# Kernel tuning notes

Hardware: AMD Instinct MI355X
Metric: run time of the kernel (lower is better)

Reference implementation:

```python
import jax, jax.numpy as jnp
import numpy as np

B, C, D, TOPK = 4096, 8192, 128, 10


def calc_distmat2(x, y):
    d = (x * x).sum(-1)[:, None] + (y * y).sum(-1)[None, :] - 2.0 * (x @ y.T)
    return jnp.clip(d, 1e-12, 1e12)


def setup_inputs() -> dict:
    key = jax.random.key(0)
    k1, k2, k3 = jax.random.split(key, 3)
    x = jax.random.normal(k1, (B, D), dtype=jnp.float32)
    labels = jax.random.randint(k2, (B,), 0, C)
    # kaiming_normal_(mode='fan_out') on (C, D): fan_out = C, gain = sqrt(2)
    centers = jax.random.normal(k3, (C, D), dtype=jnp.float32) * np.float32(np.sqrt(2.0 / C))
    return {"x": x, "labels": labels, "centers": centers, "topk": TOPK}


def reference(x, labels, centers, topk):
    num_classes = centers.shape[0]
    distmat = calc_distmat2(x, centers)                      # (B, C)
    lab = labels[:, None]                                    # (B, 1)
    dist_pull = jnp.take_along_axis(distmat, lab, axis=1)[:, 0]  # (B,)
    loss_pull = dist_pull.mean()

    # mode 'exp': per-row masked topk over negatives + log-softmax over [pos, neg_topk]
    logits = -distmat                                        # (B, C)
    pos = jnp.take_along_axis(logits, lab, axis=1)           # (B, 1)
    is_pos = lab == jnp.arange(num_classes)[None, :]         # (B, C)
    neg_logits = jnp.where(is_pos, -jnp.inf, logits)
    neg_topk, _ = jax.lax.top_k(neg_logits, topk)            # (B, topk)
    cat = jnp.concatenate([pos, neg_topk], axis=1)           # (B, 1+topk)
    # -log_softmax at index 0 (the positive) per row, averaged ('ccent')
    loss = (-jax.nn.log_softmax(cat, axis=1)[:, 0]).mean()

    # center-to-center repulsion over strictly-lower-triangular pairs
    cent2cent = calc_distmat2(centers, centers)              # (C, C)
    tri = jnp.tril(jnp.ones((num_classes, num_classes), dtype=bool), -1)
    n_pairs = num_classes * (num_classes - 1) // 2
    loss_dis = -jnp.sum(jnp.where(tri, cent2cent, 0.0)) / jnp.float32(n_pairs)

    return (loss, loss_dis, cent2cent, loss_pull)
```

## Files before the change

### kernel.cpp

```cpp
#include <hip/hip_runtime.h>
#include <hip/hip_bf16.h>
#include <math.h>

#define NB 4096
#define NC 8192
#define ND 128
#define NSPLIT 16
#define CPS (NC / NSPLIT)
#define NTILES (CPS / 16)
#define XBLKS (64 * NSPLIT)

#define WS_XN 16
#define WS_CN (WS_XN + NB)
#define WS_POS (WS_CN + NC)
#define WS_PART (WS_POS + NB)
#define WS_XB (WS_PART + NB * NSPLIT * 10)
#define WS_CB (WS_XB + NB * ND / 2)

typedef __attribute__((ext_vector_type(8))) short short8v;
typedef __attribute__((ext_vector_type(4))) float f32x4;

__global__ __launch_bounds__(256) void prep_kernel(
    const float* __restrict__ x, const float* __restrict__ c, float* __restrict__ ws) {
  if (blockIdx.x == 0 && threadIdx.x < 16) ws[threadIdx.x] = 0.0f;
  int wid = threadIdx.x >> 6, lane = threadIdx.x & 63;
  int row = blockIdx.x * 4 + wid;
  const float* src;
  float* ndst;
  ushort* bdst;
  if (row < NB) {
    src = x + (size_t)row * ND;
    ndst = ws + WS_XN + row;
    bdst = (ushort*)(ws + WS_XB) + (size_t)row * ND;
  } else {
    int r = row - NB;
    src = c + (size_t)r * ND;
    ndst = ws + WS_CN + r;
    bdst = (ushort*)(ws + WS_CB) + (size_t)r * ND;
  }
  float2 v = *(const float2*)(src + lane * 2);
  __hip_bfloat16 h0 = __float2bfloat16(v.x);
  __hip_bfloat16 h1 = __float2bfloat16(v.y);
  ushort2 u;
  u.x = *(ushort*)&h0;
  u.y = *(ushort*)&h1;
  *(ushort2*)(bdst + lane * 2) = u;
  float s = fmaf(v.x, v.x, v.y * v.y);
#pragma unroll
  for (int off = 32; off; off >>= 1) s += __shfl_down(s, off, 64);
  if (lane == 0) *ndst = s;
}

#define INS10(arr, val)                          \
  {                                              \
    float _v = (val);                            \
    _Pragma("unroll") for (int _k = 0; _k < 10; ++_k) { \
      float _mx = fmaxf(arr[_k], _v);            \
      _v = fminf(arr[_k], _v);                   \
      arr[_k] = _mx;                             \
    }                                            \
  }

__global__ __launch_bounds__(256) void mega_kernel(
    const int* __restrict__ labels, float* __restrict__ ws, float* __restrict__ outmat) {
  int t = threadIdx.x;
  int w = t >> 6, l = t & 63, lo = l & 15, hi = l >> 4;
  int bid = blockIdx.x;

  if (bid < XBLKS) {
    int split = bid >> 6;
    int row = (bid & 63) * 64 + w * 16 + lo;
    int cbase = split * CPS;
    const ushort* xb = (const ushort*)(ws + WS_XB);
    const ushort* cb = (const ushort*)(ws + WS_CB);

    const ushort* xrp = xb + (size_t)row * ND + hi * 8;
    short8v xf0 = *(const short8v*)(xrp + 0);
    short8v xf1 = *(const short8v*)(xrp + 32);
    short8v xf2 = *(const short8v*)(xrp + 64);
    short8v xf3 = *(const short8v*)(xrp + 96);

    float xn = ws[WS_XN + row];
    int lab = labels[row];

    float top[10];
#pragma unroll
    for (int k = 0; k < 10; ++k) top[k] = -3.0e38f;
    float posv = -3.0e38f;

    for (int tl = 0; tl < NTILES; ++tl) {
      int c0 = cbase + tl * 16;
      const ushort* cp = cb + (size_t)(c0 + lo) * ND + hi * 8;
      short8v a0 = *(const short8v*)(cp + 0);
      short8v a1 = *(const short8v*)(cp + 32);
      short8v a2 = *(const short8v*)(cp + 64);
      short8v a3 = *(const short8v*)(cp + 96);
      f32x4 acc = {0.f, 0.f, 0.f, 0.f};
      acc = __builtin_amdgcn_mfma_f32_16x16x32_bf16(a0, xf0, acc, 0, 0, 0);
      acc = __builtin_amdgcn_mfma_f32_16x16x32_bf16(a1, xf1, acc, 0, 0, 0);
      acc = __builtin_amdgcn_mfma_f32_16x16x32_bf16(a2, xf2, acc, 0, 0, 0);
      acc = __builtin_amdgcn_mfma_f32_16x16x32_bf16(a3, xf3, acc, 0, 0, 0);

      f32x4 cn4 = *(const f32x4*)(ws + WS_CN + c0 + hi * 4);
#pragma unroll
      for (int r = 0; r < 4; ++r) {
        int cidx = c0 + hi * 4 + r;
        float dist = xn + cn4[r] - 2.0f * acc[r];
        dist = fminf(fmaxf(dist, 1e-12f), 1e12f);
        float s = -dist;
        bool isl = (cidx == lab);
        posv = isl ? s : posv;
        float se = isl ? -3.0e38f : s;
        INS10(top, se)
      }
    }

    float oth[10];
#pragma unroll
    for (int m = 16; m <= 32; m <<= 1) {
#pragma unroll
      for (int k = 0; k < 10; ++k) oth[k] = __shfl_xor(top[k], m, 64);
#pragma unroll
      for (int k = 0; k < 10; ++k) INS10(top, oth[k])
    }

    if (posv > -1.0e37f) ws[WS_POS + row] = posv;
    if (hi == 0) {
      float* dst = ws + WS_PART + ((size_t)row * NSPLIT + split) * 10;
#pragma unroll
      for (int k = 0; k < 10; ++k) dst[k] = top[k];
    }
  } else {
    int bid2 = bid - XBLKS;
    int bi = bid2 >> 6, bj = bid2 & 63;
    int wm = w >> 1, wn = w & 1;
    int rowb = bi * 128 + wm * 64;
    int colb = bj * 128 + wn * 64;
    const ushort* cb = (const ushort*)(ws + WS_CB);

    f32x4 acc[4][4];
#pragma unroll
    for (int m = 0; m < 4; ++m)
#pragma unroll
      for (int n = 0; n < 4; ++n) acc[m][n] = (f32x4){0.f, 0.f, 0.f, 0.f};

#pragma unroll
    for (int ks = 0; ks < 4; ++ks) {
      short8v af[4], bf[4];
#pragma unroll
      for (int m = 0; m < 4; ++m)
        af[m] = *(const short8v*)(cb + (size_t)(rowb + m * 16 + lo) * ND + ks * 32 + hi * 8);
#pragma unroll
      for (int n = 0; n < 4; ++n)
        bf[n] = *(const short8v*)(cb + (size_t)(colb + n * 16 + lo) * ND + ks * 32 + hi * 8);
#pragma unroll
      for (int m = 0; m < 4; ++m)
#pragma unroll
        for (int n = 0; n < 4; ++n)
          acc[m][n] = __builtin_amdgcn_mfma_f32_16x16x32_bf16(af[m], bf[n], acc[m][n], 0, 0, 0);
    }

    float cnj[4];
#pragma unroll
    for (int n = 0; n < 4; ++n) cnj[n] = ws[WS_CN + colb + n * 16 + lo];
    float tsum = 0.0f;
#pragma unroll
    for (int m = 0; m < 4; ++m) {
      f32x4 cni = *(const f32x4*)(ws + WS_CN + rowb + m * 16 + hi * 4);
#pragma unroll
      for (int n = 0; n < 4; ++n) {
#pragma unroll
        for (int rr = 0; rr < 4; ++rr) {
          int gr = rowb + m * 16 + hi * 4 + rr;
          int gc = colb + n * 16 + lo;
          float dd = cni[rr] + cnj[n] - 2.0f * acc[m][n][rr];
          dd = fminf(fmaxf(dd, 1e-12f), 1e12f);
          outmat[(size_t)gr * NC + gc] = dd;
          if (bi > bj) tsum += dd;
          else if (bi == bj) tsum += (gr > gc) ? dd : 0.0f;
        }
      }
    }

    __shared__ float red[4];
#pragma unroll
    for (int off = 32; off; off >>= 1) tsum += __shfl_down(tsum, off, 64);
    if (l == 0) red[w] = tsum;
    __syncthreads();
    if (t == 0) atomicAdd(ws + 1, red[0] + red[1] + red[2] + red[3]);
  }
}

__global__ __launch_bounds__(256) void merge_fin_kernel(float* __restrict__ ws,
                                                        float* __restrict__ out) {
  int row = blockIdx.x * 256 + threadIdx.x;
  const f32x4* part = (const f32x4*)(ws + WS_PART + (size_t)row * NSPLIT * 10);
  float top[10];
#pragma unroll
  for (int k = 0; k < 10; ++k) top[k] = -3.0e38f;
#pragma unroll
  for (int i = 0; i < NSPLIT * 10 / 4; ++i) {
    f32x4 v = part[i];
    INS10(top, v.x)
    INS10(top, v.y)
    INS10(top, v.z)
    INS10(top, v.w)
  }
  float pos = ws[WS_POS + row];
  float mx = fmaxf(pos, top[0]);
  float ssum = expf(pos - mx);
#pragma unroll
  for (int k = 0; k < 10; ++k) ssum += expf(top[k] - mx);
  float lrow = mx + logf(ssum) - pos;
  float prow = -pos;
#pragma unroll
  for (int off = 32; off; off >>= 1) {
    lrow += __shfl_down(lrow, off, 64);
    prow += __shfl_down(prow, off, 64);
  }
  if ((threadIdx.x & 63) == 0) {
    atomicAdd(ws + 0, lrow);
    atomicAdd(ws + 2, prow);
  }
  __syncthreads();
  if (threadIdx.x == 0) {
    __threadfence();
    unsigned tk = atomicAdd((unsigned int*)(ws + 3), 1u);
    if (tk == 15u) {
      float ls = atomicAdd(ws + 0, 0.0f);
      float ts = atomicAdd(ws + 1, 0.0f);
      float ps = atomicAdd(ws + 2, 0.0f);
      out[0] = ls / 4096.0f;
      out[1] = -ts / 33550336.0f;
      out[2 + (size_t)NC * NC] = ps / 4096.0f;
    }
  }
}

extern "C" void kernel_launch(void* const* d_in, const int* in_sizes, int n_in,
                              void* d_out, int out_size, void* d_ws, size_t ws_size,
                              hipStream_t stream) {
  const float* x = (const float*)d_in[0];
  const int* labels = (const int*)d_in[1];
  const float* centers = (const float*)d_in[2];
  float* out = (float*)d_out;
  float* ws = (float*)d_ws;

  hipLaunchKernelGGL(prep_kernel, dim3((NB + NC) / 4), dim3(256), 0, stream, x, centers, ws);
  hipLaunchKernelGGL(mega_kernel, dim3(XBLKS + 64 * 64), dim3(256), 0, stream, labels, ws, out + 2);
  hipLaunchKernelGGL(merge_fin_kernel, dim3(NB / 256), dim3(256), 0, stream, ws, out);
}
```

Baseline: 182.9 us.

## Split mega kernel into c2c and xloss kernels with pipelined loads and merge-insert top-k

Splits the fused kernel into two launches: a center-to-center distance kernel and an x-loss top-k kernel, each with its own register footprint. The c2c kernel swaps MFMA operand order so each lane writes four contiguous floats, giving vectorized float4 stores of the 256MB output instead of scalar ones. The xloss kernel double-buffers center fragment loads across tiles and replaces four sequential 10-wide insertions with a 4-element sorting network merged into the top-10 list. In exchange it loses the overlap between the two workloads inside one grid and adds a kernel launch.

```diff
diff --git a/kernel.cpp b/kernel.cpp
--- a/kernel.cpp
+++ b/kernel.cpp
@@ -8,7 +8,7 @@
 #define NSPLIT 16
 #define CPS (NC / NSPLIT)
 #define NTILES (CPS / 16)
-#define XBLKS (64 * NSPLIT)
+#define NEGINF -3.0e38f
 
 #define WS_XN 16
 #define WS_CN (WS_XN + NB)
@@ -61,134 +61,193 @@
     }                                            \
   }
 
-__global__ __launch_bounds__(256) void mega_kernel(
-    const int* __restrict__ labels, float* __restrict__ ws, float* __restrict__ outmat) {
+#define SW(a, b) { float _x = fmaxf(a, b); b = fminf(a, b); a = _x; }
+
+#define LOADF(d0, d1, d2, d3, IDX)                                            \
+  {                                                                           \
+    const ushort* cp_ = cb + (size_t)(cbase + (IDX) * 16 + lo) * ND + hi * 8; \
+    d0 = *(const short8v*)(cp_ + 0);                                          \
+    d1 = *(const short8v*)(cp_ + 32);                                         \
+    d2 = *(const short8v*)(cp_ + 64);                                         \
+    d3 = *(const short8v*)(cp_ + 96);                                         \
+  }
+
+#define EPILOGUE(TL, ACC, CN4)                                                \
+  {                                                                           \
+    int cb0_ = cbase + (TL) * 16 + hi * 4;                                    \
+    float a0 = -(fminf(fmaxf(xn + (CN4).x - 2.0f * (ACC)[0], 1e-12f), 1e12f));\
+    float a1 = -(fminf(fmaxf(xn + (CN4).y - 2.0f * (ACC)[1], 1e-12f), 1e12f));\
+    float a2 = -(fminf(fmaxf(xn + (CN4).z - 2.0f * (ACC)[2], 1e-12f), 1e12f));\
+    float a3 = -(fminf(fmaxf(xn + (CN4).w - 2.0f * (ACC)[3], 1e-12f), 1e12f));\
+    bool l0 = (cb0_ + 0 == lab), l1 = (cb0_ + 1 == lab),                      \
+         l2 = (cb0_ + 2 == lab), l3 = (cb0_ + 3 == lab);                      \
+    posv = l0 ? a0 : posv; posv = l1 ? a1 : posv;                             \
+    posv = l2 ? a2 : posv; posv = l3 ? a3 : posv;                             \
+    a0 = l0 ? NEGINF : a0; a1 = l1 ? NEGINF : a1;                             \
+    a2 = l2 ? NEGINF : a2; a3 = l3 ? NEGINF : a3;                             \
+    SW(a0, a1) SW(a2, a3) SW(a0, a2) SW(a1, a3) SW(a1, a2)                    \
+    float n0 = fmaxf(a0, top[0]);                                             \
+    float n1 = fmaxf(fmaxf(a1, top[1]), fminf(a0, top[0]));                   \
+    float n2 = fmaxf(fmaxf(a2, top[2]),                                       \
+                     fmaxf(fminf(a0, top[1]), fminf(a1, top[0])));            \
+    float n3 = fmaxf(fmaxf(a3, top[3]),                                       \
+                     fmaxf(fmaxf(fminf(a0, top[2]), fminf(a1, top[1])),       \
+                           fminf(a2, top[0])));                               \
+    float n4 = fmaxf(top[4], fmaxf(fmaxf(fminf(a0, top[3]), fminf(a1, top[2])), \
+                                   fmaxf(fminf(a2, top[1]), fminf(a3, top[0])))); \
+    float n5 = fmaxf(top[5], fmaxf(fmaxf(fminf(a0, top[4]), fminf(a1, top[3])), \
+                                   fmaxf(fminf(a2, top[2]), fminf(a3, top[1])))); \
+    float n6 = fmaxf(top[6], fmaxf(fmaxf(fminf(a0, top[5]), fminf(a1, top[4])), \
+                                   fmaxf(fminf(a2, top[3]), fminf(a3, top[2])))); \
+    float n7 = fmaxf(top[7], fmaxf(fmaxf(fminf(a0, top[6]), fminf(a1, top[5])), \
+                                   fmaxf(fminf(a2, top[4]), fminf(a3, top[3])))); \
+    float n8 = fmaxf(top[8], fmaxf(fmaxf(fminf(a0, top[7]), fminf(a1, top[6])), \
+                                   fmaxf(fminf(a2, top[5]), fminf(a3, top[4])))); \
+    float n9 = fmaxf(top[9], fmaxf(fmaxf(fminf(a0, top[8]), fminf(a1, top[7])), \
+                                   fmaxf(fminf(a2, top[6]), fminf(a3, top[5])))); \
+    top[0] = n0; top[1] = n1; top[2] = n2; top[3] = n3; top[4] = n4;          \
+    top[5] = n5; top[6] = n6; top[7] = n7; top[8] = n8; top[9] = n9;          \
+  }
+
+__global__ __launch_bounds__(256) void xloss_kernel(
+    const int* __restrict__ labels, float* __restrict__ ws) {
   int t = threadIdx.x;
   int w = t >> 6, l = t & 63, lo = l & 15, hi = l >> 4;
-  int bid = blockIdx.x;
-
-  if (bid < XBLKS) {
-    int split = bid >> 6;
-    int row = (bid & 63) * 64 + w * 16 + lo;
-    int cbase = split * CPS;
-    const ushort* xb = (const ushort*)(ws + WS_XB);
-    const ushort* cb = (const ushort*)(ws + WS_CB);
-
-    const ushort* xrp = xb + (size_t)row * ND + hi * 8;
-    short8v xf0 = *(const short8v*)(xrp + 0);
-    short8v xf1 = *(const short8v*)(xrp + 32);
-    short8v xf2 = *(const short8v*)(xrp + 64);
-    short8v xf3 = *(const short8v*)(xrp + 96);
-
-    float xn = ws[WS_XN + row];
-    int lab = labels[row];
-
-    float top[10];
-#pragma unroll
-    for (int k = 0; k < 10; ++k) top[k] = -3.0e38f;
-    float posv = -3.0e38f;
-
-    for (int tl = 0; tl < NTILES; ++tl) {
-      int c0 = cbase + tl * 16;
-      const ushort* cp = cb + (size_t)(c0 + lo) * ND + hi * 8;
-      short8v a0 = *(const short8v*)(cp + 0);
-      short8v a1 = *(const short8v*)(cp + 32);
-      short8v a2 = *(const short8v*)(cp + 64);
-      short8v a3 = *(const short8v*)(cp + 96);
-      f32x4 acc = {0.f, 0.f, 0.f, 0.f};
-      acc = __builtin_amdgcn_mfma_f32_16x16x32_bf16(a0, xf0, acc, 0, 0, 0);
-      acc = __builtin_amdgcn_mfma_f32_16x16x32_bf16(a1, xf1, acc, 0, 0, 0);
-      acc = __builtin_amdgcn_mfma_f32_16x16x32_bf16(a2, xf2, acc, 0, 0, 0);
-      acc = __builtin_amdgcn_mfma_f32_16x16x32_bf16(a3, xf3, acc, 0, 0, 0);
-
-      f32x4 cn4 = *(const f32x4*)(ws + WS_CN + c0 + hi * 4);
-#pragma unroll
-      for (int r = 0; r < 4; ++r) {
-        int cidx = c0 + hi * 4 + r;
-        float dist = xn + cn4[r] - 2.0f * acc[r];
-        dist = fminf(fmaxf(dist, 1e-12f), 1e12f);
-        float s = -dist;
-        bool isl = (cidx == lab);
-        posv = isl ? s : posv;
-        float se = isl ? -3.0e38f : s;
-        INS10(top, se)
+  int row = blockIdx.x * 64 + w * 16 + lo;
+  int split = blockIdx.y;
+  int cbase = split * CPS;
+
+  const ushort* xb = (const ushort*)(ws + WS_XB);
+  const ushort* cb = (const ushort*)(ws + WS_CB);
+
+  const ushort* xrp = xb + (size_t)row * ND + hi * 8;
+  short8v xf0 = *(const short8v*)(xrp + 0);
+  short8v xf1 = *(const short8v*)(xrp + 32);
+  short8v xf2 = *(const short8v*)(xrp + 64);
+  short8v xf3 = *(const short8v*)(xrp + 96);
+
+  float xn = ws[WS_XN + row];
+  int lab = labels[row];
+
+  float top[10];
+#pragma unroll
+  for (int k = 0; k < 10; ++k) top[k] = NEGINF;
+  float posv = NEGINF;
+
+  short8v pa0, pa1, pa2, pa3, qa0, qa1, qa2, qa3;
+  f32x4 cnP, cnQ;
+  LOADF(pa0, pa1, pa2, pa3, 0)
+  cnP = *(const f32x4*)(ws + WS_CN + cbase + hi * 4);
+
+  for (int tl = 0; tl < NTILES; tl += 2) {
+    LOADF(qa0, qa1, qa2, qa3, tl + 1)
+    cnQ = *(const f32x4*)(ws + WS_CN + cbase + (tl + 1) * 16 + hi * 4);
+
+    f32x4 accA = {0.f, 0.f, 0.f, 0.f};
+    accA = __builtin_amdgcn_mfma_f32_16x16x32_bf16(pa0, xf0, accA, 0, 0, 0);
+    accA = __builtin_amdgcn_mfma_f32_16x16x32_bf16(pa1, xf1, accA, 0, 0, 0);
+    accA = __builtin_amdgcn_mfma_f32_16x16x32_bf16(pa2, xf2, accA, 0, 0, 0);
+    accA = __builtin_amdgcn_mfma_f32_16x16x32_bf16(pa3, xf3, accA, 0, 0, 0);
+    f32x4 cnA = cnP;
+    int nidx = (tl + 2 < NTILES) ? tl + 2 : tl;
+    LOADF(pa0, pa1, pa2, pa3, nidx)
+    cnP = *(const f32x4*)(ws + WS_CN + cbase + nidx * 16 + hi * 4);
+
+    EPILOGUE(tl, accA, cnA)
+
+    f32x4 accB = {0.f, 0.f, 0.f, 0.f};
+    accB = __builtin_amdgcn_mfma_f32_16x16x32_bf16(qa0, xf0, accB, 0, 0, 0);
+    accB = __builtin_amdgcn_mfma_f32_16x16x32_bf16(qa1, xf1, accB, 0, 0, 0);
+    accB = __builtin_amdgcn_mfma_f32_16x16x32_bf16(qa2, xf2, accB, 0, 0, 0);
+    accB = __builtin_amdgcn_mfma_f32_16x16x32_bf16(qa3, xf3, accB, 0, 0, 0);
+    EPILOGUE(tl + 1, accB, cnQ)
+  }
+
+  float oth[10];
+#pragma unroll
+  for (int m = 16; m <= 32; m <<= 1) {
+#pragma unroll
+    for (int k = 0; k < 10; ++k) oth[k] = __shfl_xor(top[k], m, 64);
+#pragma unroll
+    for (int k = 0; k < 10; ++k) INS10(top, oth[k])
+  }
+
+  if (posv > -1.0e37f) ws[WS_POS + row] = posv;
+  if (hi == 0) {
+    float* dst = ws + WS_PART + ((size_t)row * NSPLIT + split) * 10;
+#pragma unroll
+    for (int k = 0; k < 10; ++k) dst[k] = top[k];
+  }
+}
+
+__global__ __launch_bounds__(256) void c2c_kernel(
+    float* __restrict__ ws, float* __restrict__ outmat) {
+  int bi = blockIdx.x, bj = blockIdx.y;
+  int t = threadIdx.x;
+  int w = t >> 6, l = t & 63, lo = l & 15, hi = l >> 4;
+  int wm = w >> 1, wn = w & 1;
+  int rowb = bi * 128 + wm * 64;
+  int colb = bj * 128 + wn * 64;
+  const ushort* cb = (const ushort*)(ws + WS_CB);
+
+  f32x4 acc[4][4];
+#pragma unroll
+  for (int m = 0; m < 4; ++m)
+#pragma unroll
+    for (int n = 0; n < 4; ++n) acc[m][n] = (f32x4){0.f, 0.f, 0.f, 0.f};
+
+#pragma unroll
+  for (int ks = 0; ks < 4; ++ks) {
+    short8v af[4], bf[4];
+#pragma unroll
+    for (int m = 0; m < 4; ++m)
+      af[m] = *(const short8v*)(cb + (size_t)(rowb + m * 16 + lo) * ND + ks * 32 + hi * 8);
+#pragma unroll
+    for (int n = 0; n < 4; ++n)
+      bf[n] = *(const short8v*)(cb + (size_t)(colb + n * 16 + lo) * ND + ks * 32 + hi * 8);
+#pragma unroll
+    for (int m = 0; m < 4; ++m)
+#pragma unroll
+      for (int n = 0; n < 4; ++n)
+        acc[m][n] = __builtin_amdgcn_mfma_f32_16x16x32_bf16(bf[n], af[m], acc[m][n], 0, 0, 0);
+  }
+
+  float cni[4];
+#pragma unroll
+  for (int m = 0; m < 4; ++m) cni[m] = ws[WS_CN + rowb + m * 16 + lo];
+  f32x4 cnj[4];
+#pragma unroll
+  for (int n = 0; n < 4; ++n)
+    cnj[n] = *(const f32x4*)(ws + WS_CN + colb + n * 16 + hi * 4);
+
+  float tsum = 0.0f;
+#pragma unroll
+  for (int m = 0; m < 4; ++m) {
+    int gr = rowb + m * 16 + lo;
+    float* orow = outmat + (size_t)gr * NC + colb + hi * 4;
+#pragma unroll
+    for (int n = 0; n < 4; ++n) {
+      f32x4 dd;
+#pragma unroll
+      for (int rr = 0; rr < 4; ++rr)
+        dd[rr] = fminf(fmaxf(cni[m] + cnj[n][rr] - 2.0f * acc[m][n][rr], 1e-12f), 1e12f);
+      if (bi > bj) {
+        tsum += dd[0] + dd[1] + dd[2] + dd[3];
+      } else if (bi == bj) {
+        int gc0 = colb + n * 16 + hi * 4;
+#pragma unroll
+        for (int rr = 0; rr < 4; ++rr) tsum += (gr > gc0 + rr) ? dd[rr] : 0.0f;
       }
+      *(f32x4*)(orow + n * 16) = dd;
     }
-
-    float oth[10];
-#pragma unroll
-    for (int m = 16; m <= 32; m <<= 1) {
-#pragma unroll
-      for (int k = 0; k < 10; ++k) oth[k] = __shfl_xor(top[k], m, 64);
-#pragma unroll
-      for (int k = 0; k < 10; ++k) INS10(top, oth[k])
-    }
-
-    if (posv > -1.0e37f) ws[WS_POS + row] = posv;
-    if (hi == 0) {
-      float* dst = ws + WS_PART + ((size_t)row * NSPLIT + split) * 10;
-#pragma unroll
-      for (int k = 0; k < 10; ++k) dst[k] = top[k];
-    }
-  } else {
-    int bid2 = bid - XBLKS;
-    int bi = bid2 >> 6, bj = bid2 & 63;
-    int wm = w >> 1, wn = w & 1;
-    int rowb = bi * 128 + wm * 64;
-    int colb = bj * 128 + wn * 64;
-    const ushort* cb = (const ushort*)(ws + WS_CB);
-
-    f32x4 acc[4][4];
-#pragma unroll
-    for (int m = 0; m < 4; ++m)
-#pragma unroll
-      for (int n = 0; n < 4; ++n) acc[m][n] = (f32x4){0.f, 0.f, 0.f, 0.f};
-
-#pragma unroll
-    for (int ks = 0; ks < 4; ++ks) {
-      short8v af[4], bf[4];
-#pragma unroll
-      for (int m = 0; m < 4; ++m)
-        af[m] = *(const short8v*)(cb + (size_t)(rowb + m * 16 + lo) * ND + ks * 32 + hi * 8);
-#pragma unroll
-      for (int n = 0; n < 4; ++n)
-        bf[n] = *(const short8v*)(cb + (size_t)(colb + n * 16 + lo) * ND + ks * 32 + hi * 8);
-#pragma unroll
-      for (int m = 0; m < 4; ++m)
-#pragma unroll
-        for (int n = 0; n < 4; ++n)
-          acc[m][n] = __builtin_amdgcn_mfma_f32_16x16x32_bf16(af[m], bf[n], acc[m][n], 0, 0, 0);
-    }
-
-    float cnj[4];
-#pragma unroll
-    for (int n = 0; n < 4; ++n) cnj[n] = ws[WS_CN + colb + n * 16 + lo];
-    float tsum = 0.0f;
-#pragma unroll
-    for (int m = 0; m < 4; ++m) {
-      f32x4 cni = *(const f32x4*)(ws + WS_CN + rowb + m * 16 + hi * 4);
-#pragma unroll
-      for (int n = 0; n < 4; ++n) {
-#pragma unroll
-        for (int rr = 0; rr < 4; ++rr) {
-          int gr = rowb + m * 16 + hi * 4 + rr;
-          int gc = colb + n * 16 + lo;
-          float dd = cni[rr] + cnj[n] - 2.0f * acc[m][n][rr];
-          dd = fminf(fmaxf(dd, 1e-12f), 1e12f);
-          outmat[(size_t)gr * NC + gc] = dd;
-          if (bi > bj) tsum += dd;
-          else if (bi == bj) tsum += (gr > gc) ? dd : 0.0f;
-        }
-      }
-    }
-
-    __shared__ float red[4];
-#pragma unroll
-    for (int off = 32; off; off >>= 1) tsum += __shfl_down(tsum, off, 64);
-    if (l == 0) red[w] = tsum;
-    __syncthreads();
-    if (t == 0) atomicAdd(ws + 1, red[0] + red[1] + red[2] + red[3]);
-  }
+  }
+
+  __shared__ float red[4];
+#pragma unroll
+  for (int off = 32; off; off >>= 1) tsum += __shfl_down(tsum, off, 64);
+  if (l == 0) red[w] = tsum;
+  __syncthreads();
+  if (t == 0) atomicAdd(ws + 1, red[0] + red[1] + red[2] + red[3]);
 }
 
 __global__ __launch_bounds__(256) void merge_fin_kernel(float* __restrict__ ws,
@@ -197,7 +256,7 @@
   const f32x4* part = (const f32x4*)(ws + WS_PART + (size_t)row * NSPLIT * 10);
   float top[10];
 #pragma unroll
-  for (int k = 0; k < 10; ++k) top[k] = -3.0e38f;
+  for (int k = 0; k < 10; ++k) top[k] = NEGINF;
 #pragma unroll
   for (int i = 0; i < NSPLIT * 10 / 4; ++i) {
     f32x4 v = part[i];
@@ -247,6 +306,7 @@
   float* ws = (float*)d_ws;
 
   hipLaunchKernelGGL(prep_kernel, dim3((NB + NC) / 4), dim3(256), 0, stream, x, centers, ws);
-  hipLaunchKernelGGL(mega_kernel, dim3(XBLKS + 64 * 64), dim3(256), 0, stream, labels, ws, out + 2);
+  hipLaunchKernelGGL(c2c_kernel, dim3(64, 64), dim3(256), 0, stream, ws, out + 2);
+  hipLaunchKernelGGL(xloss_kernel, dim3(64, NSPLIT), dim3(256), 0, stream, labels, ws);
   hipLaunchKernelGGL(merge_fin_kernel, dim3(NB / 256), dim3(256), 0, stream, ws, out);
 }
```

New measurement: 179.7 us. About the same (-1.8%).
